# Kernel optimization log

Measured on AMD Instinct MI355X. Metric: run time of the kernel, lower is better.

## Reference

```python
import jax, jax.numpy as jnp
import numpy as np

B, L, D, H = 2, 2048, 1024, 16
HD = D // H
ROPE_BASE = 10000.0


def _chain_info(lengths):
    """lengths: [B, L] int, chain lengths packed at the front, zeros after.
    Returns per-position within-chain positions (RoPE resets per chain),
    chain ids, and a validity mask."""
    def one(row):
        csum = jnp.cumsum(row)                      # [L]
        total = csum[-1]
        p = jnp.arange(L)
        cid = jnp.searchsorted(csum, p, side='right')  # chain id per position
        prev = jnp.where(cid > 0, csum[jnp.clip(cid - 1, 0, L - 1)], 0)
        valid = p < total
        pos = jnp.where(valid, p - prev, 0).astype(jnp.float32)
        return pos, cid, valid
    return jax.vmap(one)(lengths)


def _rope_tables(pos):
    # pos: [B, L] float -> cos/sin [B, L, 1, HD]
    inv_freq = 1.0 / (ROPE_BASE ** (jnp.arange(0, HD, 2, dtype=jnp.float32) / HD))
    freqs = pos[..., None] * inv_freq               # [B, L, HD/2]
    emb = jnp.concatenate([freqs, freqs], axis=-1)  # [B, L, HD]
    return jnp.cos(emb)[:, :, None, :], jnp.sin(emb)[:, :, None, :]


def _apply_rope(x, cos, sin):
    d = x.shape[-1]
    x1, x2 = x[..., : d // 2], x[..., d // 2:]
    return x * cos + jnp.concatenate([-x2, x1], axis=-1) * sin


def _branch(x, Wqkv, bqkv, cos, sin, allowed):
    # x: [B, L, D]; allowed: [B, L, L] bool attention mask for this branch
    qkv = x @ Wqkv.T + bqkv                          # [B, L, 3D]
    qkv = qkv.reshape(B, L, 3, H, HD)
    q, k, v = qkv[:, :, 0], qkv[:, :, 1], qkv[:, :, 2]
    q = q * (HD ** -0.5)
    q = _apply_rope(q, cos, sin)
    k = _apply_rope(k, cos, sin)
    scores = jnp.einsum('bthd,bshd->bhts', q, k)     # [B, H, L, L]
    scores = jnp.where(allowed[:, None], scores, -jnp.inf)
    probs = jax.nn.softmax(scores, axis=-1)
    probs = jnp.where(jnp.isnan(probs), 0.0, probs)  # fully-masked rows -> 0
    out = jnp.einsum('bhts,bshd->bthd', probs, v)    # [B, L, H, HD]
    return out.reshape(B, L, D)


def setup_inputs() -> dict:
    key = jax.random.key(0)
    ks = jax.random.split(key, 7)
    s = 0.02
    lens = np.zeros((B, L), np.int64)
    lens[0, :8] = [300, 250, 200, 400, 350, 248, 150, 100]   # sum 1998
    lens[1, :6] = [512, 400, 300, 360, 276, 200]             # sum 2048
    return {
        'hidden_states': jax.random.normal(ks[0], (B, L, D), jnp.float32),
        'attention_mask_in_length': jnp.asarray(lens),
        'Wqkv_intra': jax.random.normal(ks[1], (3 * D, D), jnp.float32) * s,
        'bqkv_intra': jnp.zeros((3 * D,), jnp.float32),
        'Wqkv_inter': jax.random.normal(ks[2], (3 * D, D), jnp.float32) * s,
        'bqkv_inter': jnp.zeros((3 * D,), jnp.float32),
        'Wout': jax.random.normal(ks[3], (D, D), jnp.float32) * s,
        'bout': jnp.zeros((D,), jnp.float32),
    }


def reference(hidden_states, attention_mask_in_length, Wqkv_intra, bqkv_intra,
              Wqkv_inter, bqkv_inter, Wout, bout):
    pos, cid, valid = _chain_info(attention_mask_in_length)
    cos, sin = _rope_tables(pos)
    same_chain = cid[:, :, None] == cid[:, None, :]          # [B, L, L]
    key_valid = valid[:, None, :]                            # [B, 1, L]
    allowed_intra = same_chain & key_valid
    allowed_inter = (~same_chain) & key_valid
    out_intra = _branch(hidden_states, Wqkv_intra, bqkv_intra, cos, sin, allowed_intra)
    out_inter = _branch(hidden_states, Wqkv_inter, bqkv_inter, cos, sin, allowed_inter)
    return (out_intra + out_inter) @ Wout.T + bout
```

## Files before the change

kernel.cpp:

```cpp
#include <hip/hip_runtime.h>
#include <hip/hip_bf16.h>
#include <stdint.h>

#define B 2
#define L 2048
#define D 1024
#define H 16
#define HD 64
#define NT (L / 64)
#define INVALID_CID 0x40000000

typedef __hip_bfloat16 bf16;
typedef __attribute__((ext_vector_type(8))) short short8;
typedef __attribute__((ext_vector_type(4))) float floatx4;
typedef __attribute__((ext_vector_type(4))) unsigned int uint4v;

static __device__ __forceinline__ short f2bf(float f) {
    bf16 h = __float2bfloat16(f);
    return *reinterpret_cast<short*>(&h);
}

static __device__ __forceinline__ void async_copy16(const void* g, void* l) {
    __builtin_amdgcn_global_load_lds((__attribute__((address_space(1))) void*)g,
                                     (__attribute__((address_space(3))) void*)l,
                                     16, 0, 0);
}

__global__ void chain_kernel(const int* __restrict__ lens,
                             float* __restrict__ pos, int* __restrict__ cid,
                             int4* __restrict__ tinfo)
{
    __shared__ int csum[L];
    __shared__ int cids[L];
    __shared__ int part[256];
    int b = blockIdx.x;
    int t = threadIdx.x;

    int loc[8];
    int s = 0;
    #pragma unroll
    for (int j = 0; j < 8; ++j) { s += lens[b * L + t * 8 + j]; loc[j] = s; }
    part[t] = s;
    __syncthreads();
    if (t == 0) {
        int acc = 0;
        for (int i = 0; i < 256; ++i) { int v = part[i]; part[i] = acc; acc += v; }
    }
    __syncthreads();
    int base = part[t];
    #pragma unroll
    for (int j = 0; j < 8; ++j) csum[t * 8 + j] = base + loc[j];
    __syncthreads();

    int total = csum[L - 1];
    for (int p = t; p < L; p += 256) {
        int cv;
        if (p < total) {
            int lo = 0, hi = L;
            while (lo < hi) {
                int mid = (lo + hi) >> 1;
                if (csum[mid] <= p) lo = mid + 1; else hi = mid;
            }
            int prev = (lo > 0) ? csum[lo - 1] : 0;
            pos[b * L + p] = (float)(p - prev);
            cv = lo;
        } else {
            pos[b * L + p] = 0.f;
            cv = INVALID_CID;
        }
        cids[p] = cv;
        cid[b * L + p] = cv;
    }
    __syncthreads();
    if (t < NT) {
        int mn = 0x7fffffff, mx = -1, any = 0, all = 1;
        for (int j = 0; j < 64; ++j) {
            int cv = cids[t * 64 + j];
            if (cv != INVALID_CID) { any = 1; mn = min(mn, cv); mx = max(mx, cv); }
            else all = 0;
        }
        tinfo[b * NT + t] = make_int4(mn, mx, any | (all << 1), 0);
    }
}

__global__ void cast_all(const float* __restrict__ x,  const float* __restrict__ Wi,
                         const float* __restrict__ We, const float* __restrict__ Wo,
                         bf16* __restrict__ xb, bf16* __restrict__ Wib,
                         bf16* __restrict__ Web, bf16* __restrict__ Wob)
{
    int bid = blockIdx.x;
    const float* src; bf16* dst; int base;
    if      (bid < 4096)  { src = x;  dst = xb;  base = bid; }
    else if (bid < 7168)  { src = Wi; dst = Wib; base = bid - 4096; }
    else if (bid < 10240) { src = We; dst = Web; base = bid - 7168; }
    else                  { src = Wo; dst = Wob; base = bid - 10240; }
    int i = (base * 256 + threadIdx.x) * 4;
    float4 v = *(const float4*)(src + i);
    dst[i + 0] = __float2bfloat16(v.x);
    dst[i + 1] = __float2bfloat16(v.y);
    dst[i + 2] = __float2bfloat16(v.z);
    dst[i + 3] = __float2bfloat16(v.w);
}

__global__ __launch_bounds__(256, 4) void gemm128(
    const bf16* __restrict__ A, const bf16* __restrict__ Bw,
    const float* __restrict__ bias, void* __restrict__ Cout,
    int M, int N, int K, int c_bf16)
{
    __shared__ short As[128 * 32];
    __shared__ short Bs[128 * 32];

    int tid = threadIdx.x;
    int wave = tid >> 6, lane = tid & 63;
    int i15 = lane & 15, q8 = lane >> 4;
    int wm = wave & 1, wn = wave >> 1;
    int m0 = blockIdx.y * 128, n0 = blockIdx.x * 128;

    floatx4 acc[4][4];
    #pragma unroll
    for (int mt = 0; mt < 4; ++mt)
        #pragma unroll
        for (int nt = 0; nt < 4; ++nt) acc[mt][nt] = (floatx4){0.f, 0.f, 0.f, 0.f};

    const short* gA = (const short*)A  + (size_t)(m0 + wave * 32 + (lane >> 2)) * K + (lane & 3) * 8;
    const short* gB = (const short*)Bw + (size_t)(n0 + wave * 32 + (lane >> 2)) * K + (lane & 3) * 8;
    short* lA = As + wave * 1024;
    short* lB = Bs + wave * 1024;

    for (int kt = 0; kt < K; kt += 32) {
        __syncthreads();
        async_copy16(gA + kt,          lA);
        async_copy16(gA + 16 * K + kt, lA + 512);
        async_copy16(gB + kt,          lB);
        async_copy16(gB + 16 * K + kt, lB + 512);
        __syncthreads();

        short8 af[4], bfr[4];
        #pragma unroll
        for (int mt = 0; mt < 4; ++mt)
            af[mt] = *(const short8*)&As[(wm * 64 + mt * 16 + i15) * 32 + q8 * 8];
        #pragma unroll
        for (int nt = 0; nt < 4; ++nt)
            bfr[nt] = *(const short8*)&Bs[(wn * 64 + nt * 16 + i15) * 32 + q8 * 8];
        #pragma unroll
        for (int mt = 0; mt < 4; ++mt)
            #pragma unroll
            for (int nt = 0; nt < 4; ++nt)
                acc[mt][nt] = __builtin_amdgcn_mfma_f32_16x16x32_bf16(af[mt], bfr[nt], acc[mt][nt], 0, 0, 0);
    }

    #pragma unroll
    for (int nt = 0; nt < 4; ++nt) {
        int n = n0 + wn * 64 + nt * 16 + i15;
        float bv = bias[n];
        #pragma unroll
        for (int mt = 0; mt < 4; ++mt) {
            #pragma unroll
            for (int rg = 0; rg < 4; ++rg) {
                int m = m0 + wm * 64 + mt * 16 + q8 * 4 + rg;
                float v = acc[mt][nt][rg] + bv;
                if (c_bf16) ((bf16*)Cout)[(size_t)m * N + n] = __float2bfloat16(v);
                else        ((float*)Cout)[(size_t)m * N + n] = v;
            }
        }
    }
}

__global__ __launch_bounds__(256) void rope_scatter2(
    const bf16* __restrict__ qkv, const float* __restrict__ pos,
    bf16* __restrict__ Qo, bf16* __restrict__ Ko, bf16* __restrict__ Vtg)
{
    __shared__ float Vsh[64][65];
    int tid = threadIdx.x;
    int bid = blockIdx.x;
    int lt = bid & (NT - 1);
    int h  = (bid >> 5) & (H - 1);
    int b  = bid >> 9;
    int l0 = lt * 64;

    const float QSCALE = 0.18033688011111772f;
    int hd = tid & 63, lq = tid >> 6;
    float sgn = (hd < 32) ? -1.f : 1.f;
    float invf = exp2f(-(float)(hd & 31) * (13.287712379549449f / 32.f));

    #pragma unroll
    for (int rr = 0; rr < 16; ++rr) {
        int l = l0 + lq * 16 + rr;
        size_t row = (size_t)(b * L + l) * (3 * D);
        int col  = h * HD + hd;
        int col2 = h * HD + (hd ^ 32);

        float xq  = __bfloat162float(qkv[row + col]);
        float xq2 = __bfloat162float(qkv[row + col2]);
        float xk  = __bfloat162float(qkv[row + D + col]);
        float xk2 = __bfloat162float(qkv[row + D + col2]);
        float xv  = __bfloat162float(qkv[row + 2 * D + col]);

        float p = pos[b * L + l];
        float ang = p * invf;
        float cc = cosf(ang), ss = sinf(ang);

        float qo = QSCALE * (xq * cc + sgn * xq2 * ss);
        float ko = xk * cc + sgn * xk2 * ss;

        size_t o = ((size_t)(b * H + h) * L + l) * HD + hd;
        Qo[o] = __float2bfloat16(qo);
        Ko[o] = __float2bfloat16(ko);
        Vsh[l - l0][hd] = xv;
    }
    __syncthreads();
    int lcol = tid & 63, dq = tid >> 6;
    #pragma unroll
    for (int rr = 0; rr < 16; ++rr) {
        int dd = dq * 16 + rr;
        Vtg[((size_t)(b * H + h) * HD + dd) * L + l0 + lcol] = __float2bfloat16(Vsh[lcol][dd]);
    }
}

__global__ __launch_bounds__(256, 4) void attn5(
    const bf16* __restrict__ Q, const bf16* __restrict__ Kg, const bf16* __restrict__ Vtg,
    const int* __restrict__ cid, const int4* __restrict__ tinfo,
    float* __restrict__ OutF, bf16* __restrict__ OutB, const float* __restrict__ Prev,
    int branch)
{
    __shared__ short Ks[2][64][72];
    __shared__ short Vs[2][64][72];
    __shared__ int cls_s[NT];
    __shared__ int list_s[NT];
    __shared__ int nlist_s;

    int tid = threadIdx.x;
    int wave = tid >> 6, lane = tid & 63;
    int i15 = lane & 15, q8 = lane >> 4;
    int workid = ((blockIdx.x & 7) << 7) | (blockIdx.x >> 3);
    int qt = workid & (NT - 1);
    int h  = (workid >> 5) & (H - 1);
    int b  = workid >> 9;
    int q0 = qt * 64;
    const size_t bh  = (size_t)(b * H + h) * L;
    const size_t bhd = (size_t)(b * H + h) * HD;

    short8 qf[2];
    {
        const short* qp = (const short*)Q + (bh + q0 + wave * 16 + i15) * HD + q8 * 8;
        qf[0] = *(const short8*)(qp);
        qf[1] = *(const short8*)(qp + 32);
    }
    int cq = cid[b * L + q0 + wave * 16 + i15];

    int4 qinf = tinfo[b * NT + qt];
    int qall = (qinf.z >> 1) & 1;

    if (tid < NT) {
        int4 ki = tinfo[b * NT + tid];
        int kany = ki.z & 1, kall = (ki.z >> 1) & 1;
        bool disjoint = (ki.x > qinf.y) || (ki.y < qinf.x);
        bool mono = qall && kall && (qinf.x == qinf.y) && (ki.x == ki.y) && (qinf.x == ki.x);
        int cls;
        if (branch == 0) {
            if (!kany || disjoint) cls = 0;
            else if (mono) cls = 2;
            else cls = 1;
        } else {
            if (!kany || mono) cls = 0;
            else if (kall && disjoint) cls = 2;
            else cls = 1;
        }
        cls_s[tid] = cls;
    }
    __syncthreads();
    if (tid == 0) {
        int n = 0;
        for (int t = 0; t < NT; ++t) {
            int c = cls_s[t];
            if (c) list_s[n++] = (t * 64) | ((c == 2) << 16);
        }
        nlist_s = n;
    }
    __syncthreads();
    int n = nlist_s;

    int r = tid >> 2, ccol = (tid & 3) * 16;
    int sr = ((((r >> 2) & 1) | ((r >> 5) << 1)) << 4) | (((r >> 3) & 3) << 2) | (r & 3);
    const short* Kbase = (const short*)Kg  + (bh + r) * HD + ccol;
    const short* Vbase = (const short*)Vtg + (bhd + r) * L + ccol;

    int4 pk0, pk1, pv0, pv1;
    int cur = 0;
    if (n > 0) {
        cur = list_s[0];
        int kt0 = cur & 0xffff;
        pk0 = *(const int4*)(Kbase + (size_t)kt0 * HD);
        pk1 = *(const int4*)(Kbase + (size_t)kt0 * HD + 8);
        pv0 = *(const int4*)(Vbase + kt0);
        pv1 = *(const int4*)(Vbase + kt0 + 8);
    }

    floatx4 accO[4];
    #pragma unroll
    for (int t = 0; t < 4; ++t) accO[t] = (floatx4){0.f, 0.f, 0.f, 0.f};
    float lsum = 0.f;

    for (int i = 0; i < n; ++i) {
        int kt = cur & 0xffff, full = cur >> 16;
        int buf = i & 1;

        *(int4*)&Ks[buf][sr][ccol]     = pk0;
        *(int4*)&Ks[buf][sr][ccol + 8] = pk1;
        *(int4*)&Vs[buf][r][ccol]      = pv0;
        *(int4*)&Vs[buf][r][ccol + 8]  = pv1;
        __syncthreads();

        if (i + 1 < n) {
            cur = list_s[i + 1];
            int nk = cur & 0xffff;
            pk0 = *(const int4*)(Kbase + (size_t)nk * HD);
            pk1 = *(const int4*)(Kbase + (size_t)nk * HD + 8);
            pv0 = *(const int4*)(Vbase + nk);
            pv1 = *(const int4*)(Vbase + nk + 8);
        }

        unsigned int dl[4], dh[4];
        #pragma unroll
        for (int t = 0; t < 4; ++t) {
            floatx4 accS = (floatx4){0.f, 0.f, 0.f, 0.f};
            short8 b0 = *(const short8*)&Ks[buf][t * 16 + i15][q8 * 8];
            short8 b1 = *(const short8*)&Ks[buf][t * 16 + i15][32 + q8 * 8];
            accS = __builtin_amdgcn_mfma_f32_16x16x32_bf16(b0, qf[0], accS, 0, 0, 0);
            accS = __builtin_amdgcn_mfma_f32_16x16x32_bf16(b1, qf[1], accS, 0, 0, 0);

            if (!full) {
                int4 ck4 = *(const int4*)(cid + b * L + kt + (q8 << 3) + ((t & 1) << 2) + ((t >> 1) << 5));
                int ckr[4] = {ck4.x, ck4.y, ck4.z, ck4.w};
                #pragma unroll
                for (int rg = 0; rg < 4; ++rg) {
                    bool kv = (ckr[rg] != INVALID_CID);
                    bool match = (cq == ckr[rg]);
                    bool ok = kv && (branch ? !match : match);
                    accS[rg] = ok ? accS[rg] : -1e30f;
                }
            }

            float p0 = __builtin_amdgcn_exp2f(accS[0]);
            float p1 = __builtin_amdgcn_exp2f(accS[1]);
            float p2 = __builtin_amdgcn_exp2f(accS[2]);
            float p3 = __builtin_amdgcn_exp2f(accS[3]);
            lsum += (p0 + p1) + (p2 + p3);
            dl[t] = (unsigned int)(unsigned short)f2bf(p0) | ((unsigned int)(unsigned short)f2bf(p1) << 16);
            dh[t] = (unsigned int)(unsigned short)f2bf(p2) | ((unsigned int)(unsigned short)f2bf(p3) << 16);
        }

        union { uint4v u; short8 s; } pa0, pa1;
        pa0.u = (uint4v){dl[0], dh[0], dl[1], dh[1]};
        pa1.u = (uint4v){dl[2], dh[2], dl[3], dh[3]};

        #pragma unroll
        for (int dt = 0; dt < 4; ++dt) {
            short8 vf0 = *(const short8*)&Vs[buf][dt * 16 + i15][q8 * 8];
            short8 vf1 = *(const short8*)&Vs[buf][dt * 16 + i15][32 + q8 * 8];
            accO[dt] = __builtin_amdgcn_mfma_f32_16x16x32_bf16(pa0.s, vf0, accO[dt], 0, 0, 0);
            accO[dt] = __builtin_amdgcn_mfma_f32_16x16x32_bf16(pa1.s, vf1, accO[dt], 0, 0, 0);
        }
    }

    lsum += __shfl_xor(lsum, 16, 64);
    lsum += __shfl_xor(lsum, 32, 64);
    float inv[4];
    #pragma unroll
    for (int rg = 0; rg < 4; ++rg) {
        float ls = __shfl(lsum, q8 * 4 + rg, 64);
        inv[rg] = (ls > 0.f) ? 1.f / ls : 0.f;
    }

    #pragma unroll
    for (int t = 0; t < 4; ++t) {
        #pragma unroll
        for (int rg = 0; rg < 4; ++rg) {
            size_t idx = (size_t)(b * L + q0 + wave * 16 + q8 * 4 + rg) * D + h * HD + t * 16 + i15;
            float o = accO[t][rg] * inv[rg];
            if (branch == 0) OutF[idx] = o;
            else             OutB[idx] = __float2bfloat16(o + Prev[idx]);
        }
    }
}

extern "C" void kernel_launch(void* const* d_in, const int* in_sizes, int n_in,
                              void* d_out, int out_size, void* d_ws, size_t ws_size,
                              hipStream_t stream)
{
    const float* x    = (const float*)d_in[0];
    const int*   mlen = (const int*)  d_in[1];
    const float* Wi   = (const float*)d_in[2];
    const float* bi   = (const float*)d_in[3];
    const float* We   = (const float*)d_in[4];
    const float* be   = (const float*)d_in[5];
    const float* Wo   = (const float*)d_in[6];
    const float* bo   = (const float*)d_in[7];

    char* ws = (char*)d_ws;
    size_t off = 0;
    auto alloc = [&](size_t bytes) {
        void* p = ws + off;
        off += (bytes + 255) & ~(size_t)255;
        return p;
    };
    bf16*  x_b   = (bf16*) alloc((size_t)B * L * D * 2);
    bf16*  Wi_b  = (bf16*) alloc((size_t)3 * D * D * 2);
    bf16*  We_b  = (bf16*) alloc((size_t)3 * D * D * 2);
    bf16*  Wo_b  = (bf16*) alloc((size_t)D * D * 2);
    bf16*  qkv_b = (bf16*) alloc((size_t)B * L * 3 * D * 2);
    bf16*  q_b   = (bf16*) alloc((size_t)B * H * L * HD * 2);
    bf16*  k_b   = (bf16*) alloc((size_t)B * H * L * HD * 2);
    bf16*  vt_b  = (bf16*) alloc((size_t)B * H * HD * L * 2);
    float* att_i = (float*)alloc((size_t)B * L * D * 4);
    bf16*  sum_b = (bf16*) alloc((size_t)B * L * D * 2);
    float* pos   = (float*)alloc((size_t)B * L * 4);
    int*   cid   = (int*)  alloc((size_t)B * L * 4);
    int4*  tinfo = (int4*) alloc((size_t)B * NT * 16);
    (void)ws_size; (void)n_in; (void)in_sizes; (void)out_size;

    chain_kernel<<<B, 256, 0, stream>>>(mlen, pos, cid, tinfo);

    cast_all<<<11264, 256, 0, stream>>>(x, Wi, We, Wo, x_b, Wi_b, We_b, Wo_b);

    dim3 gq(3 * D / 128, B * L / 128);
    gemm128<<<gq, 256, 0, stream>>>(x_b, Wi_b, bi, qkv_b, B * L, 3 * D, D, 1);
    rope_scatter2<<<B * H * NT, 256, 0, stream>>>(qkv_b, pos, q_b, k_b, vt_b);
    attn5<<<B * H * NT, 256, 0, stream>>>(q_b, k_b, vt_b, cid, tinfo, att_i, sum_b, att_i, 0);

    gemm128<<<gq, 256, 0, stream>>>(x_b, We_b, be, qkv_b, B * L, 3 * D, D, 1);
    rope_scatter2<<<B * H * NT, 256, 0, stream>>>(qkv_b, pos, q_b, k_b, vt_b);
    attn5<<<B * H * NT, 256, 0, stream>>>(q_b, k_b, vt_b, cid, tinfo, att_i, sum_b, att_i, 1);

    dim3 go(D / 128, B * L / 128);
    gemm128<<<go, 256, 0, stream>>>(sum_b, Wo_b, bo, d_out, B * L, D, D, 0);
}
```

Before: 337.3 us.

## Merge both QKV GEMMs into one and process 128 query rows per attention block

The intra and inter QKV projections now run as a single GEMM with N=6D. This relies on the two bf16 weight buffers sitting next to each other in the workspace, and it uses a split bias so each half gets its own bias. The attention kernel now handles two 64-row query groups per block, so each loaded K/V tile serves twice as many queries, and the grid is halved. The trade-offs: tile classification now uses the merged range of the two query tiles, so fewer tiles can be skipped or take the unmasked path, and fewer blocks with more registers each lowers occupancy.

```diff
diff --git a/kernel.cpp b/kernel.cpp
--- a/kernel.cpp
+++ b/kernel.cpp
@@ -8,6 +8,7 @@
 #define H 16
 #define HD 64
 #define NT (L / 64)
+#define NQT (L / 128)
 #define INVALID_CID 0x40000000
 
 typedef __hip_bfloat16 bf16;
@@ -104,8 +105,8 @@
 
 __global__ __launch_bounds__(256, 4) void gemm128(
     const bf16* __restrict__ A, const bf16* __restrict__ Bw,
-    const float* __restrict__ bias, void* __restrict__ Cout,
-    int M, int N, int K, int c_bf16)
+    const float* __restrict__ bias, const float* __restrict__ bias2,
+    void* __restrict__ Cout, int M, int N, int K, int c_bf16, int nsplit)
 {
     __shared__ short As[128 * 32];
     __shared__ short Bs[128 * 32];
@@ -152,7 +153,7 @@
     #pragma unroll
     for (int nt = 0; nt < 4; ++nt) {
         int n = n0 + wn * 64 + nt * 16 + i15;
-        float bv = bias[n];
+        float bv = (n < nsplit) ? bias[n] : bias2[n - nsplit];
         #pragma unroll
         for (int mt = 0; mt < 4; ++mt) {
             #pragma unroll
@@ -167,7 +168,7 @@
 }
 
 __global__ __launch_bounds__(256) void rope_scatter2(
-    const bf16* __restrict__ qkv, const float* __restrict__ pos,
+    const bf16* __restrict__ qkv, int rowstride, const float* __restrict__ pos,
     bf16* __restrict__ Qo, bf16* __restrict__ Ko, bf16* __restrict__ Vtg)
 {
     __shared__ float Vsh[64][65];
@@ -186,7 +187,7 @@
     #pragma unroll
     for (int rr = 0; rr < 16; ++rr) {
         int l = l0 + lq * 16 + rr;
-        size_t row = (size_t)(b * L + l) * (3 * D);
+        size_t row = (size_t)(b * L + l) * rowstride;
         int col  = h * HD + hd;
         int col2 = h * HD + (hd ^ 32);
 
@@ -217,7 +218,7 @@
     }
 }
 
-__global__ __launch_bounds__(256, 4) void attn5(
+__global__ __launch_bounds__(256, 2) void attn6(
     const bf16* __restrict__ Q, const bf16* __restrict__ Kg, const bf16* __restrict__ Vtg,
     const int* __restrict__ cid, const int4* __restrict__ tinfo,
     float* __restrict__ OutF, bf16* __restrict__ OutB, const float* __restrict__ Prev,
@@ -232,23 +233,30 @@
     int tid = threadIdx.x;
     int wave = tid >> 6, lane = tid & 63;
     int i15 = lane & 15, q8 = lane >> 4;
-    int workid = ((blockIdx.x & 7) << 7) | (blockIdx.x >> 3);
-    int qt = workid & (NT - 1);
-    int h  = (workid >> 5) & (H - 1);
-    int b  = workid >> 9;
-    int q0 = qt * 64;
+    int workid = ((blockIdx.x & 7) << 6) | (blockIdx.x >> 3);
+    int qt = workid & (NQT - 1);
+    int h  = (workid >> 4) & (H - 1);
+    int b  = workid >> 8;
+    int q0 = qt * 128;
     const size_t bh  = (size_t)(b * H + h) * L;
     const size_t bhd = (size_t)(b * H + h) * HD;
 
-    short8 qf[2];
-    {
-        const short* qp = (const short*)Q + (bh + q0 + wave * 16 + i15) * HD + q8 * 8;
-        qf[0] = *(const short8*)(qp);
-        qf[1] = *(const short8*)(qp + 32);
-    }
-    int cq = cid[b * L + q0 + wave * 16 + i15];
-
-    int4 qinf = tinfo[b * NT + qt];
+    short8 qf[2][2];
+    int cq[2];
+    #pragma unroll
+    for (int g = 0; g < 2; ++g) {
+        const short* qp = (const short*)Q + (bh + q0 + g * 64 + wave * 16 + i15) * HD + q8 * 8;
+        qf[g][0] = *(const short8*)(qp);
+        qf[g][1] = *(const short8*)(qp + 32);
+        cq[g] = cid[b * L + q0 + g * 64 + wave * 16 + i15];
+    }
+
+    int4 qa = tinfo[b * NT + 2 * qt];
+    int4 qb4 = tinfo[b * NT + 2 * qt + 1];
+    int4 qinf;
+    qinf.x = min(qa.x, qb4.x);
+    qinf.y = max(qa.y, qb4.y);
+    qinf.z = ((qa.z | qb4.z) & 1) | (qa.z & qb4.z & 2);
     int qall = (qinf.z >> 1) & 1;
 
     if (tid < NT) {
@@ -296,10 +304,12 @@
         pv1 = *(const int4*)(Vbase + kt0 + 8);
     }
 
-    floatx4 accO[4];
-    #pragma unroll
-    for (int t = 0; t < 4; ++t) accO[t] = (floatx4){0.f, 0.f, 0.f, 0.f};
-    float lsum = 0.f;
+    floatx4 accO[2][4];
+    #pragma unroll
+    for (int g = 0; g < 2; ++g)
+        #pragma unroll
+        for (int t = 0; t < 4; ++t) accO[g][t] = (floatx4){0.f, 0.f, 0.f, 0.f};
+    float lsum[2] = {0.f, 0.f};
 
     for (int i = 0; i < n; ++i) {
         int kt = cur & 0xffff, full = cur >> 16;
@@ -320,66 +330,85 @@
             pv1 = *(const int4*)(Vbase + nk + 8);
         }
 
-        unsigned int dl[4], dh[4];
+        unsigned int dl[2][4], dh[2][4];
         #pragma unroll
         for (int t = 0; t < 4; ++t) {
-            floatx4 accS = (floatx4){0.f, 0.f, 0.f, 0.f};
             short8 b0 = *(const short8*)&Ks[buf][t * 16 + i15][q8 * 8];
             short8 b1 = *(const short8*)&Ks[buf][t * 16 + i15][32 + q8 * 8];
-            accS = __builtin_amdgcn_mfma_f32_16x16x32_bf16(b0, qf[0], accS, 0, 0, 0);
-            accS = __builtin_amdgcn_mfma_f32_16x16x32_bf16(b1, qf[1], accS, 0, 0, 0);
+
+            floatx4 accS[2];
+            #pragma unroll
+            for (int g = 0; g < 2; ++g) {
+                accS[g] = (floatx4){0.f, 0.f, 0.f, 0.f};
+                accS[g] = __builtin_amdgcn_mfma_f32_16x16x32_bf16(b0, qf[g][0], accS[g], 0, 0, 0);
+                accS[g] = __builtin_amdgcn_mfma_f32_16x16x32_bf16(b1, qf[g][1], accS[g], 0, 0, 0);
+            }
 
             if (!full) {
                 int4 ck4 = *(const int4*)(cid + b * L + kt + (q8 << 3) + ((t & 1) << 2) + ((t >> 1) << 5));
                 int ckr[4] = {ck4.x, ck4.y, ck4.z, ck4.w};
                 #pragma unroll
-                for (int rg = 0; rg < 4; ++rg) {
-                    bool kv = (ckr[rg] != INVALID_CID);
-                    bool match = (cq == ckr[rg]);
-                    bool ok = kv && (branch ? !match : match);
-                    accS[rg] = ok ? accS[rg] : -1e30f;
-                }
-            }
-
-            float p0 = __builtin_amdgcn_exp2f(accS[0]);
-            float p1 = __builtin_amdgcn_exp2f(accS[1]);
-            float p2 = __builtin_amdgcn_exp2f(accS[2]);
-            float p3 = __builtin_amdgcn_exp2f(accS[3]);
-            lsum += (p0 + p1) + (p2 + p3);
-            dl[t] = (unsigned int)(unsigned short)f2bf(p0) | ((unsigned int)(unsigned short)f2bf(p1) << 16);
-            dh[t] = (unsigned int)(unsigned short)f2bf(p2) | ((unsigned int)(unsigned short)f2bf(p3) << 16);
-        }
-
-        union { uint4v u; short8 s; } pa0, pa1;
-        pa0.u = (uint4v){dl[0], dh[0], dl[1], dh[1]};
-        pa1.u = (uint4v){dl[2], dh[2], dl[3], dh[3]};
+                for (int g = 0; g < 2; ++g)
+                    #pragma unroll
+                    for (int rg = 0; rg < 4; ++rg) {
+                        bool kv = (ckr[rg] != INVALID_CID);
+                        bool match = (cq[g] == ckr[rg]);
+                        bool ok = kv && (branch ? !match : match);
+                        accS[g][rg] = ok ? accS[g][rg] : -1e30f;
+                    }
+            }
+
+            #pragma unroll
+            for (int g = 0; g < 2; ++g) {
+                float p0 = __builtin_amdgcn_exp2f(accS[g][0]);
+                float p1 = __builtin_amdgcn_exp2f(accS[g][1]);
+                float p2 = __builtin_amdgcn_exp2f(accS[g][2]);
+                float p3 = __builtin_amdgcn_exp2f(accS[g][3]);
+                lsum[g] += (p0 + p1) + (p2 + p3);
+                dl[g][t] = (unsigned int)(unsigned short)f2bf(p0) | ((unsigned int)(unsigned short)f2bf(p1) << 16);
+                dh[g][t] = (unsigned int)(unsigned short)f2bf(p2) | ((unsigned int)(unsigned short)f2bf(p3) << 16);
+            }
+        }
+
+        union { uint4v u; short8 s; } pa0[2], pa1[2];
+        #pragma unroll
+        for (int g = 0; g < 2; ++g) {
+            pa0[g].u = (uint4v){dl[g][0], dh[g][0], dl[g][1], dh[g][1]};
+            pa1[g].u = (uint4v){dl[g][2], dh[g][2], dl[g][3], dh[g][3]};
+        }
 
         #pragma unroll
         for (int dt = 0; dt < 4; ++dt) {
             short8 vf0 = *(const short8*)&Vs[buf][dt * 16 + i15][q8 * 8];
             short8 vf1 = *(const short8*)&Vs[buf][dt * 16 + i15][32 + q8 * 8];
-            accO[dt] = __builtin_amdgcn_mfma_f32_16x16x32_bf16(pa0.s, vf0, accO[dt], 0, 0, 0);
-            accO[dt] = __builtin_amdgcn_mfma_f32_16x16x32_bf16(pa1.s, vf1, accO[dt], 0, 0, 0);
-        }
-    }
-
-    lsum += __shfl_xor(lsum, 16, 64);
-    lsum += __shfl_xor(lsum, 32, 64);
-    float inv[4];
-    #pragma unroll
-    for (int rg = 0; rg < 4; ++rg) {
-        float ls = __shfl(lsum, q8 * 4 + rg, 64);
-        inv[rg] = (ls > 0.f) ? 1.f / ls : 0.f;
-    }
-
-    #pragma unroll
-    for (int t = 0; t < 4; ++t) {
+            #pragma unroll
+            for (int g = 0; g < 2; ++g) {
+                accO[g][dt] = __builtin_amdgcn_mfma_f32_16x16x32_bf16(pa0[g].s, vf0, accO[g][dt], 0, 0, 0);
+                accO[g][dt] = __builtin_amdgcn_mfma_f32_16x16x32_bf16(pa1[g].s, vf1, accO[g][dt], 0, 0, 0);
+            }
+        }
+    }
+
+    #pragma unroll
+    for (int g = 0; g < 2; ++g) {
+        float ls = lsum[g];
+        ls += __shfl_xor(ls, 16, 64);
+        ls += __shfl_xor(ls, 32, 64);
+        float inv[4];
         #pragma unroll
         for (int rg = 0; rg < 4; ++rg) {
-            size_t idx = (size_t)(b * L + q0 + wave * 16 + q8 * 4 + rg) * D + h * HD + t * 16 + i15;
-            float o = accO[t][rg] * inv[rg];
-            if (branch == 0) OutF[idx] = o;
-            else             OutB[idx] = __float2bfloat16(o + Prev[idx]);
+            float lv = __shfl(ls, q8 * 4 + rg, 64);
+            inv[rg] = (lv > 0.f) ? 1.f / lv : 0.f;
+        }
+        #pragma unroll
+        for (int t = 0; t < 4; ++t) {
+            #pragma unroll
+            for (int rg = 0; rg < 4; ++rg) {
+                size_t idx = (size_t)(b * L + q0 + g * 64 + wave * 16 + q8 * 4 + rg) * D + h * HD + t * 16 + i15;
+                float o = accO[g][t][rg] * inv[rg];
+                if (branch == 0) OutF[idx] = o;
+                else             OutB[idx] = __float2bfloat16(o + Prev[idx]);
+            }
         }
     }
 }
@@ -408,7 +437,7 @@
     bf16*  Wi_b  = (bf16*) alloc((size_t)3 * D * D * 2);
     bf16*  We_b  = (bf16*) alloc((size_t)3 * D * D * 2);
     bf16*  Wo_b  = (bf16*) alloc((size_t)D * D * 2);
-    bf16*  qkv_b = (bf16*) alloc((size_t)B * L * 3 * D * 2);
+    bf16*  qkv_b = (bf16*) alloc((size_t)B * L * 6 * D * 2);
     bf16*  q_b   = (bf16*) alloc((size_t)B * H * L * HD * 2);
     bf16*  k_b   = (bf16*) alloc((size_t)B * H * L * HD * 2);
     bf16*  vt_b  = (bf16*) alloc((size_t)B * H * HD * L * 2);
@@ -423,15 +452,15 @@
 
     cast_all<<<11264, 256, 0, stream>>>(x, Wi, We, Wo, x_b, Wi_b, We_b, Wo_b);
 
-    dim3 gq(3 * D / 128, B * L / 128);
-    gemm128<<<gq, 256, 0, stream>>>(x_b, Wi_b, bi, qkv_b, B * L, 3 * D, D, 1);
-    rope_scatter2<<<B * H * NT, 256, 0, stream>>>(qkv_b, pos, q_b, k_b, vt_b);
-    attn5<<<B * H * NT, 256, 0, stream>>>(q_b, k_b, vt_b, cid, tinfo, att_i, sum_b, att_i, 0);
-
-    gemm128<<<gq, 256, 0, stream>>>(x_b, We_b, be, qkv_b, B * L, 3 * D, D, 1);
-    rope_scatter2<<<B * H * NT, 256, 0, stream>>>(qkv_b, pos, q_b, k_b, vt_b);
-    attn5<<<B * H * NT, 256, 0, stream>>>(q_b, k_b, vt_b, cid, tinfo, att_i, sum_b, att_i, 1);
+    dim3 gq(6 * D / 128, B * L / 128);
+    gemm128<<<gq, 256, 0, stream>>>(x_b, Wi_b, bi, be, qkv_b, B * L, 6 * D, D, 1, 3 * D);
+
+    rope_scatter2<<<B * H * NT, 256, 0, stream>>>(qkv_b,         6 * D, pos, q_b, k_b, vt_b);
+    attn6<<<B * H * NQT, 256, 0, stream>>>(q_b, k_b, vt_b, cid, tinfo, att_i, sum_b, att_i, 0);
+
+    rope_scatter2<<<B * H * NT, 256, 0, stream>>>(qkv_b + 3 * D, 6 * D, pos, q_b, k_b, vt_b);
+    attn6<<<B * H * NQT, 256, 0, stream>>>(q_b, k_b, vt_b, cid, tinfo, att_i, sum_b, att_i, 1);
 
     dim3 go(D / 128, B * L / 128);
-    gemm128<<<go, 256, 0, stream>>>(sum_b, Wo_b, bo, d_out, B * L, D, D, 0);
-}
+    gemm128<<<go, 256, 0, stream>>>(sum_b, Wo_b, bo, bo, d_out, B * L, D, D, 0, D);
+}
```

Result: no change. 331.8 us (-1.6%).
